# Optimization experiments

Hardware: AMD Instinct MI355X
Metric: run time of the kernel (lower is better)

The kernel has to match this reference:

```python
import jax, jax.numpy as jnp
import numpy as np

H = 1024   # hidden_size
S = 32768  # seq_len


def setup_inputs() -> dict:
    key = jax.random.key(0)
    k1, k2, k3, k4 = jax.random.split(key, 4)
    scale = 1.0 / np.sqrt(H)
    return {
        "hidden": jax.random.normal(k1, (H,), dtype=jnp.float32),
        "encoder_outputs": jax.random.normal(k2, (S, H), dtype=jnp.float32),
        "W": jax.random.normal(k3, (H, H), dtype=jnp.float32) * scale,
        "b": jax.random.normal(k4, (H,), dtype=jnp.float32) * scale,
    }


def reference(hidden, encoder_outputs, W, b):
    # method == 'general': energy_i = W @ enc_i + b ; score_i = hidden . energy_i
    # Vectorized: scores = (enc @ W^T + b) @ hidden  -> [S]
    energies = jnp.einsum("sh,dh->sd", encoder_outputs, W) + b  # [S, H]
    scores = energies @ hidden                                   # [S]
    attn = jax.nn.softmax(scores)                                 # softmax over seq_len
    return attn[None, None, :]                                    # [1, 1, S]
```

## Files before the change

### kernel.cpp

```cpp
#include <hip/hip_runtime.h>
#include <math.h>

#define H 1024
#define S 32768
#define NPART 16
#define RPW 4
#define NB2 2048

#define WS_PART   0
#define WS_V      16384
#define WS_PM     17408
#define WS_PS     19456
#define WS_SCORES 21504

__global__ __launch_bounds__(256) void matvec_partial(const float* __restrict__ W,
                                                      const float* __restrict__ hidden,
                                                      float* __restrict__ ws) {
    float* part = ws + WS_PART;
    const int t  = threadIdx.x;
    const int l  = t & 63;
    const int dg = t >> 6;
    const int h  = blockIdx.x * 64 + l;
    const int d0 = blockIdx.y * 64 + dg * 16;

    float acc = 0.f;
#pragma unroll
    for (int i = 0; i < 16; ++i)
        acc += W[(size_t)(d0 + i) * H + h] * hidden[d0 + i];

    __shared__ float red[4][64];
    red[dg][l] = acc;
    __syncthreads();
    if (t < 64)
        part[blockIdx.y * H + blockIdx.x * 64 + l] =
            red[0][l] + red[1][l] + red[2][l] + red[3][l];
}

__device__ __forceinline__ float4 add4(float4 a, float4 b) {
    return make_float4(a.x + b.x, a.y + b.y, a.z + b.z, a.w + b.w);
}

__global__ __launch_bounds__(64) void reduce_v(float* __restrict__ ws) {
    const float* part = ws + WS_PART;
    float* v = ws + WS_V;
    const int i = blockIdx.x * 64 + threadIdx.x;
    const float4* p4 = (const float4*)part;

    float4 t[NPART];
#pragma unroll
    for (int p = 0; p < NPART; ++p) t[p] = p4[p * (H / 4) + i];
#pragma unroll
    for (int p = 0; p < 8; ++p) t[p] = add4(t[p], t[p + 8]);
#pragma unroll
    for (int p = 0; p < 4; ++p) t[p] = add4(t[p], t[p + 4]);
    t[0] = add4(add4(t[0], t[2]), add4(t[1], t[3]));
    ((float4*)v)[i] = t[0];
}

__device__ __forceinline__ float dot16(const float4 e0, const float4 e1,
                                       const float4 e2, const float4 e3,
                                       const float4 vf[4]) {
    float s0 = e0.x * vf[0].x + e0.y * vf[0].y + e0.z * vf[0].z + e0.w * vf[0].w;
    float s1 = e1.x * vf[1].x + e1.y * vf[1].y + e1.z * vf[1].z + e1.w * vf[1].w;
    float s2 = e2.x * vf[2].x + e2.y * vf[2].y + e2.z * vf[2].z + e2.w * vf[2].w;
    float s3 = e3.x * vf[3].x + e3.y * vf[3].y + e3.z * vf[3].z + e3.w * vf[3].w;
    return (s0 + s1) + (s2 + s3);
}

__global__ __launch_bounds__(256) void scores_partial(const float* __restrict__ enc,
                                                      float* __restrict__ ws) {
    float* scores = ws + WS_SCORES;
    float* pm     = ws + WS_PM;
    float* ps     = ws + WS_PS;
    const float* v = ws + WS_V;

    const int tid  = threadIdx.x;
    const int lane = tid & 63;
    const int wv   = tid >> 6;
    const int blk  = blockIdx.x;
    const int gw   = blk * 4 + wv;
    const size_t row0 = (size_t)gw * RPW;

    const float4* v4 = (const float4*)v;
    float4 vf[4];
#pragma unroll
    for (int k = 0; k < 4; ++k) vf[k] = v4[lane + 64 * k];

    float a[RPW];
#pragma unroll
    for (int it = 0; it < RPW; ++it) {
        const float4* e4 = (const float4*)(enc + (row0 + it) * H);
        a[it] = dot16(e4[lane], e4[lane + 64], e4[lane + 128], e4[lane + 192], vf);
    }

#pragma unroll
    for (int it = 0; it < RPW; ++it) {
#pragma unroll
        for (int off = 32; off > 0; off >>= 1)
            a[it] += __shfl_xor(a[it], off, 64);
    }
    if (lane == 0)
        *(float4*)(scores + row0) = make_float4(a[0], a[1], a[2], a[3]);

    const float mw = fmaxf(fmaxf(a[0], a[1]), fmaxf(a[2], a[3]));
    float sw = __expf(a[0] - mw) + __expf(a[1] - mw) +
               __expf(a[2] - mw) + __expf(a[3] - mw);

    __shared__ float sm[4], ss[4];
    if (lane == 0) { sm[wv] = mw; ss[wv] = sw; }
    __syncthreads();
    if (tid == 0) {
        float m = sm[0], s = ss[0];
#pragma unroll
        for (int i = 1; i < 4; ++i) {
            const float nm = fmaxf(m, sm[i]);
            s = s * __expf(m - nm) + ss[i] * __expf(sm[i] - nm);
            m = nm;
        }
        pm[blk] = m; ps[blk] = s;
    }
}

__global__ __launch_bounds__(256) void finalize(const float* __restrict__ ws,
                                                float* __restrict__ out) {
    const float* scores = ws + WS_SCORES;
    const float* pm     = ws + WS_PM;
    const float* ps     = ws + WS_PS;

    const int tid  = threadIdx.x;
    const int lane = tid & 63;
    const int wv   = tid >> 6;

    float m = -INFINITY, s = 0.f;
#pragma unroll
    for (int i = 0; i < NB2 / 256; ++i) {
        const int idx = tid + i * 256;
        const float om = pm[idx], os = ps[idx];
        const float nm = fmaxf(m, om);
        s = s * __expf(m - nm) + os * __expf(om - nm);
        m = nm;
    }
#pragma unroll
    for (int off = 32; off > 0; off >>= 1) {
        const float om = __shfl_xor(m, off, 64);
        const float os = __shfl_xor(s, off, 64);
        const float nm = fmaxf(m, om);
        s = s * __expf(m - nm) + os * __expf(om - nm);
        m = nm;
    }
    __shared__ float sm[4], ss[4];
    if (lane == 0) { sm[wv] = m; ss[wv] = s; }
    __syncthreads();
    float M = sm[0], Ssum = ss[0];
#pragma unroll
    for (int i = 1; i < 4; ++i) {
        const float nm = fmaxf(M, sm[i]);
        Ssum = Ssum * __expf(M - nm) + ss[i] * __expf(sm[i] - nm);
        M = nm;
    }
    const float rs = 1.0f / Ssum;

    const int i = blockIdx.x * 256 + tid;
    out[i] = __expf(scores[i] - M) * rs;
}

extern "C" void kernel_launch(void* const* d_in, const int* in_sizes, int n_in,
                              void* d_out, int out_size, void* d_ws, size_t ws_size,
                              hipStream_t stream) {
    const float* hidden = (const float*)d_in[0];
    const float* enc    = (const float*)d_in[1];
    const float* W      = (const float*)d_in[2];
    float* out = (float*)d_out;
    float* ws  = (float*)d_ws;

    matvec_partial<<<dim3(16, 16), 256, 0, stream>>>(W, hidden, ws);
    reduce_v<<<4, 64, 0, stream>>>(ws);
    scores_partial<<<NB2, 256, 0, stream>>>(enc, ws);
    finalize<<<S / 256, 256, 0, stream>>>(ws, out);
}
```

Before: 204.1 us.

## Fuse v reduction into scores kernel and double rows per wave

Removes the separate reduce_v launch by having each scores block reduce the 16 partial matvec slices into shared memory itself. The first two encoder rows are prefetched before that reduction so their loads overlap it. Rows per wave go from 4 to 8, halving the block count. In exchange every block redundantly reads the 64KB of partials (mostly from cache), and the wider per-wave work lowers parallelism.

```diff
diff --git a/kernel.cpp b/kernel.cpp
--- a/kernel.cpp
+++ b/kernel.cpp
@@ -4,14 +4,13 @@
 #define H 1024
 #define S 32768
 #define NPART 16
-#define RPW 4
-#define NB2 2048
+#define RPW 8
+#define NB2 1024
 
 #define WS_PART   0
-#define WS_V      16384
-#define WS_PM     17408
-#define WS_PS     19456
-#define WS_SCORES 21504
+#define WS_PM     16384
+#define WS_PS     17408
+#define WS_SCORES 18432
 
 __global__ __launch_bounds__(256) void matvec_partial(const float* __restrict__ W,
                                                       const float* __restrict__ hidden,
@@ -40,23 +39,6 @@
     return make_float4(a.x + b.x, a.y + b.y, a.z + b.z, a.w + b.w);
 }
 
-__global__ __launch_bounds__(64) void reduce_v(float* __restrict__ ws) {
-    const float* part = ws + WS_PART;
-    float* v = ws + WS_V;
-    const int i = blockIdx.x * 64 + threadIdx.x;
-    const float4* p4 = (const float4*)part;
-
-    float4 t[NPART];
-#pragma unroll
-    for (int p = 0; p < NPART; ++p) t[p] = p4[p * (H / 4) + i];
-#pragma unroll
-    for (int p = 0; p < 8; ++p) t[p] = add4(t[p], t[p + 8]);
-#pragma unroll
-    for (int p = 0; p < 4; ++p) t[p] = add4(t[p], t[p + 4]);
-    t[0] = add4(add4(t[0], t[2]), add4(t[1], t[3]));
-    ((float4*)v)[i] = t[0];
-}
-
 __device__ __forceinline__ float dot16(const float4 e0, const float4 e1,
                                        const float4 e2, const float4 e3,
                                        const float4 vf[4]) {
@@ -72,7 +54,7 @@
     float* scores = ws + WS_SCORES;
     float* pm     = ws + WS_PM;
     float* ps     = ws + WS_PS;
-    const float* v = ws + WS_V;
+    const float* part = ws + WS_PART;
 
     const int tid  = threadIdx.x;
     const int lane = tid & 63;
@@ -81,16 +63,38 @@
     const int gw   = blk * 4 + wv;
     const size_t row0 = (size_t)gw * RPW;
 
-    const float4* v4 = (const float4*)v;
+    const float4* e4 = (const float4*)(enc + row0 * H);
+    float4 p00 = e4[lane],       p01 = e4[lane + 64],
+           p02 = e4[lane + 128], p03 = e4[lane + 192];
+    float4 p10 = e4[256 + lane],       p11 = e4[256 + lane + 64],
+           p12 = e4[256 + lane + 128], p13 = e4[256 + lane + 192];
+
+    __shared__ float vsh[H];
+    {
+        const float4* p4 = (const float4*)part;
+        float4 t[NPART];
+#pragma unroll
+        for (int p = 0; p < NPART; ++p) t[p] = p4[p * (H / 4) + tid];
+#pragma unroll
+        for (int p = 0; p < 8; ++p) t[p] = add4(t[p], t[p + 8]);
+#pragma unroll
+        for (int p = 0; p < 4; ++p) t[p] = add4(t[p], t[p + 4]);
+        ((float4*)vsh)[tid] = add4(add4(t[0], t[2]), add4(t[1], t[3]));
+    }
+    __syncthreads();
+
+    const float4* v4 = (const float4*)vsh;
     float4 vf[4];
 #pragma unroll
     for (int k = 0; k < 4; ++k) vf[k] = v4[lane + 64 * k];
 
     float a[RPW];
+    a[0] = dot16(p00, p01, p02, p03, vf);
+    a[1] = dot16(p10, p11, p12, p13, vf);
 #pragma unroll
-    for (int it = 0; it < RPW; ++it) {
-        const float4* e4 = (const float4*)(enc + (row0 + it) * H);
-        a[it] = dot16(e4[lane], e4[lane + 64], e4[lane + 128], e4[lane + 192], vf);
+    for (int it = 2; it < RPW; ++it) {
+        const float4* r = e4 + it * 256;
+        a[it] = dot16(r[lane], r[lane + 64], r[lane + 128], r[lane + 192], vf);
     }
 
 #pragma unroll
@@ -99,12 +103,17 @@
         for (int off = 32; off > 0; off >>= 1)
             a[it] += __shfl_xor(a[it], off, 64);
     }
-    if (lane == 0)
-        *(float4*)(scores + row0) = make_float4(a[0], a[1], a[2], a[3]);
+    if (lane == 0) {
+        *(float4*)(scores + row0)     = make_float4(a[0], a[1], a[2], a[3]);
+        *(float4*)(scores + row0 + 4) = make_float4(a[4], a[5], a[6], a[7]);
+    }
 
-    const float mw = fmaxf(fmaxf(a[0], a[1]), fmaxf(a[2], a[3]));
-    float sw = __expf(a[0] - mw) + __expf(a[1] - mw) +
-               __expf(a[2] - mw) + __expf(a[3] - mw);
+    float m01 = fmaxf(a[0], a[1]), m23 = fmaxf(a[2], a[3]);
+    float m45 = fmaxf(a[4], a[5]), m67 = fmaxf(a[6], a[7]);
+    const float mw = fmaxf(fmaxf(m01, m23), fmaxf(m45, m67));
+    float sw = 0.f;
+#pragma unroll
+    for (int it = 0; it < RPW; ++it) sw += __expf(a[it] - mw);
 
     __shared__ float sm[4], ss[4];
     if (lane == 0) { sm[wv] = mw; ss[wv] = sw; }
@@ -174,7 +183,6 @@
     float* ws  = (float*)d_ws;
 
     matvec_partial<<<dim3(16, 16), 256, 0, stream>>>(W, hidden, ws);
-    reduce_v<<<4, 64, 0, stream>>>(ws);
     scores_partial<<<NB2, 256, 0, stream>>>(enc, ws);
     finalize<<<S / 256, 256, 0, stream>>>(ws, out);
 }
```

After: 201.3 us. No clear change (-1.4%).

## Fuse partial-sum reduction of v into scores kernel and preload encoder rows

Applied to the files above, without the earlier changes.

Removes the separate reduce_v launch: every scores_partial block now sums the 16 partial matvec slices into shared memory itself. All 16 float4 encoder loads per lane are also issued up front, before the v reduction result is consumed, to increase memory-level parallelism, and launch bounds request 4 blocks per CU. The cost is that 2048 blocks each reread the 64KB partial buffer, which should mostly hit in L2, plus a block barrier and higher register pressure.

```diff
diff --git a/kernel.cpp b/kernel.cpp
--- a/kernel.cpp
+++ b/kernel.cpp
@@ -8,10 +8,9 @@
 #define NB2 2048
 
 #define WS_PART   0
-#define WS_V      16384
-#define WS_PM     17408
-#define WS_PS     19456
-#define WS_SCORES 21504
+#define WS_PM     16384
+#define WS_PS     18432
+#define WS_SCORES 20480
 
 __global__ __launch_bounds__(256) void matvec_partial(const float* __restrict__ W,
                                                       const float* __restrict__ hidden,
@@ -40,39 +39,12 @@
     return make_float4(a.x + b.x, a.y + b.y, a.z + b.z, a.w + b.w);
 }
 
-__global__ __launch_bounds__(64) void reduce_v(float* __restrict__ ws) {
-    const float* part = ws + WS_PART;
-    float* v = ws + WS_V;
-    const int i = blockIdx.x * 64 + threadIdx.x;
-    const float4* p4 = (const float4*)part;
-
-    float4 t[NPART];
-#pragma unroll
-    for (int p = 0; p < NPART; ++p) t[p] = p4[p * (H / 4) + i];
-#pragma unroll
-    for (int p = 0; p < 8; ++p) t[p] = add4(t[p], t[p + 8]);
-#pragma unroll
-    for (int p = 0; p < 4; ++p) t[p] = add4(t[p], t[p + 4]);
-    t[0] = add4(add4(t[0], t[2]), add4(t[1], t[3]));
-    ((float4*)v)[i] = t[0];
-}
-
-__device__ __forceinline__ float dot16(const float4 e0, const float4 e1,
-                                       const float4 e2, const float4 e3,
-                                       const float4 vf[4]) {
-    float s0 = e0.x * vf[0].x + e0.y * vf[0].y + e0.z * vf[0].z + e0.w * vf[0].w;
-    float s1 = e1.x * vf[1].x + e1.y * vf[1].y + e1.z * vf[1].z + e1.w * vf[1].w;
-    float s2 = e2.x * vf[2].x + e2.y * vf[2].y + e2.z * vf[2].z + e2.w * vf[2].w;
-    float s3 = e3.x * vf[3].x + e3.y * vf[3].y + e3.z * vf[3].z + e3.w * vf[3].w;
-    return (s0 + s1) + (s2 + s3);
-}
-
-__global__ __launch_bounds__(256) void scores_partial(const float* __restrict__ enc,
-                                                      float* __restrict__ ws) {
+__global__ __launch_bounds__(256, 4) void scores_partial(const float* __restrict__ enc,
+                                                         float* __restrict__ ws) {
     float* scores = ws + WS_SCORES;
     float* pm     = ws + WS_PM;
     float* ps     = ws + WS_PS;
-    const float* v = ws + WS_V;
+    const float* part = ws + WS_PART;
 
     const int tid  = threadIdx.x;
     const int lane = tid & 63;
@@ -81,7 +53,29 @@
     const int gw   = blk * 4 + wv;
     const size_t row0 = (size_t)gw * RPW;
 
-    const float4* v4 = (const float4*)v;
+    __shared__ float vsh[H];
+    {
+        const float4* p4 = (const float4*)part;
+        float4 t[NPART];
+#pragma unroll
+        for (int p = 0; p < NPART; ++p) t[p] = p4[p * (H / 4) + tid];
+#pragma unroll
+        for (int p = 0; p < 8; ++p) t[p] = add4(t[p], t[p + 8]);
+#pragma unroll
+        for (int p = 0; p < 4; ++p) t[p] = add4(t[p], t[p + 4]);
+        ((float4*)vsh)[tid] = add4(add4(t[0], t[2]), add4(t[1], t[3]));
+    }
+    __syncthreads();
+
+    const float4* e4 = (const float4*)(enc + row0 * H);
+    float4 r[16];
+#pragma unroll
+    for (int it = 0; it < RPW; ++it)
+#pragma unroll
+        for (int k = 0; k < 4; ++k)
+            r[it * 4 + k] = e4[it * 256 + k * 64 + lane];
+
+    const float4* v4 = (const float4*)vsh;
     float4 vf[4];
 #pragma unroll
     for (int k = 0; k < 4; ++k) vf[k] = v4[lane + 64 * k];
@@ -89,8 +83,13 @@
     float a[RPW];
 #pragma unroll
     for (int it = 0; it < RPW; ++it) {
-        const float4* e4 = (const float4*)(enc + (row0 + it) * H);
-        a[it] = dot16(e4[lane], e4[lane + 64], e4[lane + 128], e4[lane + 192], vf);
+        const float4 e0 = r[it * 4 + 0], e1 = r[it * 4 + 1];
+        const float4 e2 = r[it * 4 + 2], e3 = r[it * 4 + 3];
+        float s0 = e0.x * vf[0].x + e0.y * vf[0].y + e0.z * vf[0].z + e0.w * vf[0].w;
+        float s1 = e1.x * vf[1].x + e1.y * vf[1].y + e1.z * vf[1].z + e1.w * vf[1].w;
+        float s2 = e2.x * vf[2].x + e2.y * vf[2].y + e2.z * vf[2].z + e2.w * vf[2].w;
+        float s3 = e3.x * vf[3].x + e3.y * vf[3].y + e3.z * vf[3].z + e3.w * vf[3].w;
+        a[it] = (s0 + s1) + (s2 + s3);
     }
 
 #pragma unroll
@@ -174,7 +173,6 @@
     float* ws  = (float*)d_ws;
 
     matvec_partial<<<dim3(16, 16), 256, 0, stream>>>(W, hidden, ws);
-    reduce_v<<<4, 64, 0, stream>>>(ws);
     scores_partial<<<NB2, 256, 0, stream>>>(enc, ws);
     finalize<<<S / 256, 256, 0, stream>>>(ws, out);
 }
```

Result: no change. 200.4 us (-1.8%).
